# Kernel tuning notes

Measured on AMD Instinct MI355X. Metric: run time of the kernel, lower is better.

The kernel has to match this reference:

```python
import jax, jax.numpy as jnp
import numpy as np

N_NODES = 100000
N_EDGES = 1600000
D_FEAT = 32


def setup_inputs() -> dict:
    key = jax.random.key(0)
    k1, k2, k3 = jax.random.split(key, 3)
    features = jax.random.normal(k1, (N_NODES, D_FEAT), dtype=jnp.float32)
    src = jax.random.randint(k2, (N_EDGES,), 0, N_NODES, dtype=jnp.int64)
    dst = jax.random.randint(k3, (N_EDGES,), 0, N_NODES, dtype=jnp.int64)
    return {"features": features, "src": src, "dst": dst}


def reference(features, src, dst):
    # LightConv with norm='both' (default): symmetric degree normalization.
    n = features.shape[0]
    # out-degrees (number of edges leaving each node)
    deg = jnp.zeros((n,), dtype=features.dtype).at[src].add(1.0)
    # norm = deg^-0.5 with inf -> 0 for isolated nodes
    norm = jnp.where(deg > 0, jax.lax.rsqrt(jnp.maximum(deg, 1.0)), 0.0)[:, None]  # [N,1]
    # pre-scale (norm in ['left','both'])
    x = features * norm
    # message = copy_src, reduce = sum over incoming edges
    agg = jax.ops.segment_sum(x[src], dst, num_segments=n)  # [N,D]
    # post-scale (norm in ['right','both']) -- original reads srcdata['norm'],
    # which is the same per-node norm array for a homogeneous graph.
    return agg * norm
```

## Files before the change

### kernel.cpp

```cpp
#include <hip/hip_runtime.h>

#define D_FEAT 32
#define NPB 256
#define NPB_SHIFT 8
#define KMAX 512
#define BPART 512
#define TPART 256
#define SRC_BITS 17
#define SRC_MASK 0x1FFFF
#define CAPI 6144
#define CAP 2048


__global__ __launch_bounds__(TPART) void partition_atomic(const int* __restrict__ src,
                                                          const int* __restrict__ dst,
                                                          int* __restrict__ cntD_g,
                                                          int* __restrict__ cntS_g,
                                                          int* __restrict__ routed_d,
                                                          unsigned char* __restrict__ routed_b,
                                                          int n_edges, int K) {
    __shared__ int hD[KMAX];
    __shared__ int hS[KMAX];
    __shared__ int bD[KMAX];
    __shared__ int bS[KMAX];
    int b = blockIdx.x;
    int tid = threadIdx.x;
    for (int i = tid; i < K; i += TPART) { hD[i] = 0; hS[i] = 0; }
    __syncthreads();
    int chunk = (((n_edges + BPART - 1) / BPART) + 3) & ~3;
    int base = b * chunk;
    int eend = min(base + chunk, n_edges);
    int nvec = (eend > base) ? ((eend - base) >> 2) : 0;
    const int4* d4p = (const int4*)(dst + base);
    const int4* s4p = (const int4*)(src + base);
    for (int i = tid; i < nvec; i += TPART) {
        int4 d4 = d4p[i];
        int4 s4 = s4p[i];
        atomicAdd(&hD[d4.x >> NPB_SHIFT], 1);
        atomicAdd(&hD[d4.y >> NPB_SHIFT], 1);
        atomicAdd(&hD[d4.z >> NPB_SHIFT], 1);
        atomicAdd(&hD[d4.w >> NPB_SHIFT], 1);
        atomicAdd(&hS[s4.x >> NPB_SHIFT], 1);
        atomicAdd(&hS[s4.y >> NPB_SHIFT], 1);
        atomicAdd(&hS[s4.z >> NPB_SHIFT], 1);
        atomicAdd(&hS[s4.w >> NPB_SHIFT], 1);
    }
    for (int e = base + nvec * 4 + tid; e < eend; e += TPART) {
        atomicAdd(&hD[dst[e] >> NPB_SHIFT], 1);
        atomicAdd(&hS[src[e] >> NPB_SHIFT], 1);
    }
    __syncthreads();
    for (int i = tid; i < K; i += TPART) {
        int c = hD[i];
        bD[i] = (c > 0) ? atomicAdd(&cntD_g[i], c) : 0;
        int c2 = hS[i];
        bS[i] = (c2 > 0) ? atomicAdd(&cntS_g[i], c2) : 0;
    }
    __syncthreads();
    for (int i = tid; i < nvec; i += TPART) {
        int4 d4 = d4p[i];
        int4 s4 = s4p[i];
        int dv[4] = {d4.x, d4.y, d4.z, d4.w};
        int sv[4] = {s4.x, s4.y, s4.z, s4.w};
        #pragma unroll
        for (int u = 0; u < 4; u++) {
            int d = dv[u], s = sv[u];
            int kd = d >> NPB_SHIFT;
            int pos = atomicAdd(&bD[kd], 1);
            routed_d[(size_t)kd * CAPI + min(pos, CAPI - 1)] = ((d & (NPB - 1)) << SRC_BITS) | s;
            int ks = s >> NPB_SHIFT;
            int ps = atomicAdd(&bS[ks], 1);
            routed_b[(size_t)ks * CAPI + min(ps, CAPI - 1)] = (unsigned char)(s & (NPB - 1));
        }
    }
    for (int e = base + nvec * 4 + tid; e < eend; e += TPART) {
        int d = dst[e], s = src[e];
        int kd = d >> NPB_SHIFT;
        int pos = atomicAdd(&bD[kd], 1);
        routed_d[(size_t)kd * CAPI + min(pos, CAPI - 1)] = ((d & (NPB - 1)) << SRC_BITS) | s;
        int ks = s >> NPB_SHIFT;
        int ps = atomicAdd(&bS[ks], 1);
        routed_b[(size_t)ks * CAPI + min(ps, CAPI - 1)] = (unsigned char)(s & (NPB - 1));
    }
}

__global__ __launch_bounds__(256) void count_norm(const unsigned char* __restrict__ routed_b,
                                                  const int* __restrict__ cntS_g,
                                                  float* __restrict__ norm,
                                                  int n_nodes, int K) {
    __shared__ int bins[NPB];
    int k = blockIdx.x;
    int tid = threadIdx.x;
    bins[tid] = 0;
    __syncthreads();
    int beg = k * CAPI;
    int cnt = min(cntS_g[k], CAPI);
    for (int j = tid; j < cnt; j += 256)
        atomicAdd(&bins[routed_b[beg + j]], 1);
    __syncthreads();
    int node = (k << NPB_SHIFT) + tid;
    if (node < n_nodes) {
        int d = bins[tid];
        norm[node] = d > 0 ? rsqrtf((float)d) : 0.0f;
    }
}

__global__ __launch_bounds__(1024) void fused_gather(const float4* __restrict__ feat4,
                                                     const int* __restrict__ routed_d,
                                                     const int* __restrict__ cntD_g,
                                                     const float* __restrict__ norm,
                                                     float4* __restrict__ out4,
                                                     int n_nodes, int K) {
    __shared__ int sbuf[CAP];
    __shared__ int ssort[CAP];
    __shared__ int bins[NPB];
    __shared__ int sc[NPB];
    __shared__ int off[NPB + 1];
    __shared__ int cur[NPB];
    int k = blockIdx.x;
    int tid = threadIdx.x;
    int g = tid >> 5;
    int lane = tid & 31;
    int sub = lane >> 3;
    int il  = lane & 7;
    int kbase = k << NPB_SHIFT;

    int beg = k * CAPI;
    int total = min(cntD_g[k], CAPI);

    float4 acc[8];
    #pragma unroll
    for (int ii = 0; ii < 8; ii++) acc[ii] = make_float4(0.f, 0.f, 0.f, 0.f);

    for (int cb = 0; cb < total; cb += CAP) {
        int n = min(CAP, total - cb);
        __syncthreads();
        for (int i = tid; i < n; i += 1024) sbuf[i] = routed_d[beg + cb + i];
        if (tid < NPB) bins[tid] = 0;
        __syncthreads();
        for (int i = tid; i < n; i += 1024) atomicAdd(&bins[sbuf[i] >> SRC_BITS], 1);
        __syncthreads();
        if (tid < NPB) sc[tid] = bins[tid];
        __syncthreads();
        for (int st = 1; st < NPB; st <<= 1) {
            int v = (tid < NPB && tid >= st) ? sc[tid - st] : 0;
            __syncthreads();
            if (tid < NPB) sc[tid] += v;
            __syncthreads();
        }
        if (tid < NPB) {
            int ex = sc[tid] - bins[tid];
            off[tid] = ex;
            cur[tid] = ex;
        }
        if (tid == NPB - 1) off[NPB] = sc[NPB - 1];
        __syncthreads();
        for (int i = tid; i < n; i += 1024) {
            int p = sbuf[i];
            int pos = atomicAdd(&cur[p >> SRC_BITS], 1);
            ssort[pos] = p & SRC_MASK;
        }
        __syncthreads();
        #pragma unroll
        for (int ii = 0; ii < 8; ii++) {
            int dl = g + (ii << 5);
            int u0 = off[dl], u1 = off[dl + 1];
            float4 a = acc[ii];
            int u = u0;
            for (; u + 8 <= u1; u += 8) {
                int s0 = ssort[u + sub];
                int s1 = ssort[u + 4 + sub];
                float4 f0 = feat4[(size_t)s0 * 8 + il];
                float4 f1 = feat4[(size_t)s1 * 8 + il];
                float w0 = norm[s0];
                float w1 = norm[s1];
                a.x += f0.x * w0 + f1.x * w1;
                a.y += f0.y * w0 + f1.y * w1;
                a.z += f0.z * w0 + f1.z * w1;
                a.w += f0.w * w0 + f1.w * w1;
            }
            for (; u < u1; u += 4) {
                if (u + sub < u1) {
                    int s = ssort[u + sub];
                    float4 f = feat4[(size_t)s * 8 + il];
                    float w = norm[s];
                    a.x += f.x * w; a.y += f.y * w; a.z += f.z * w; a.w += f.w * w;
                }
            }
            acc[ii] = a;
        }
    }

    #pragma unroll
    for (int ii = 0; ii < 8; ii++) {
        float4 a = acc[ii];
        a.x += __shfl_xor(a.x, 8, 32);  a.y += __shfl_xor(a.y, 8, 32);
        a.z += __shfl_xor(a.z, 8, 32);  a.w += __shfl_xor(a.w, 8, 32);
        a.x += __shfl_xor(a.x, 16, 32); a.y += __shfl_xor(a.y, 16, 32);
        a.z += __shfl_xor(a.z, 16, 32); a.w += __shfl_xor(a.w, 16, 32);
        int node = kbase + g + (ii << 5);
        if (node < n_nodes && lane < 8) {
            float nv = norm[node];
            a.x *= nv; a.y *= nv; a.z *= nv; a.w *= nv;
            out4[(size_t)node * 8 + il] = a;
        }
    }
}


__global__ void deg_kernel(const int* __restrict__ src, int* __restrict__ deg, int n_edges) {
    int e = blockIdx.x * blockDim.x + threadIdx.x;
    if (e < n_edges) atomicAdd(&deg[src[e]], 1);
}

__global__ void norm_kernel(const int* __restrict__ deg, float* __restrict__ norm, int n_nodes) {
    int i = blockIdx.x * blockDim.x + threadIdx.x;
    if (i < n_nodes) {
        int d = deg[i];
        norm[i] = d > 0 ? rsqrtf((float)d) : 0.0f;
    }
}

__global__ void scatter_kernel(const float* __restrict__ feat,
                               const int* __restrict__ src,
                               const int* __restrict__ dst,
                               const float* __restrict__ norm,
                               float* __restrict__ out, int n_edges) {
    int t = blockIdx.x * blockDim.x + threadIdx.x;
    int e = t >> 5;
    int d = t & 31;
    if (e < n_edges) {
        int s  = src[e];
        int dd = dst[e];
        float v = feat[s * D_FEAT + d] * norm[s];
        atomicAdd(&out[dd * D_FEAT + d], v);
    }
}

__global__ void post_scale_kernel(float4* __restrict__ out4,
                                  const float* __restrict__ norm, int n4) {
    int t = blockIdx.x * blockDim.x + threadIdx.x;
    if (t < n4) {
        float nv = norm[t >> 3];
        float4 v = out4[t];
        v.x *= nv; v.y *= nv; v.z *= nv; v.w *= nv;
        out4[t] = v;
    }
}


extern "C" void kernel_launch(void* const* d_in, const int* in_sizes, int n_in,
                              void* d_out, int out_size, void* d_ws, size_t ws_size,
                              hipStream_t stream) {
    const float* feat = (const float*)d_in[0];
    const int*   src  = (const int*)d_in[1];
    const int*   dst  = (const int*)d_in[2];
    float* out = (float*)d_out;

    const int n_nodes = in_sizes[0] / D_FEAT;
    const int n_edges = in_sizes[1];
    const int B = 256;

    const int K = (n_nodes + NPB - 1) >> NPB_SHIFT;

    auto align256 = [](size_t x) { return (x + 255) & ~(size_t)255; };
    size_t off = 0;
    size_t cnt_off    = off; off = align256(off + (size_t)2 * K * sizeof(int));
    size_t norm_off   = off; off = align256(off + (size_t)n_nodes * sizeof(float));
    size_t routd_off  = off; off = align256(off + (size_t)K * CAPI * sizeof(int));
    size_t routb_off  = off; off = align256(off + (size_t)K * CAPI * sizeof(unsigned char));
    size_t needed = off;

    bool ok = (ws_size >= needed) && (K <= KMAX) && (n_nodes <= (1 << SRC_BITS));

    if (ok) {
        int*   cntD_g          = (int*)((char*)d_ws + cnt_off);
        int*   cntS_g          = cntD_g + K;
        float* norm            = (float*)((char*)d_ws + norm_off);
        int*   routed_d        = (int*)((char*)d_ws + routd_off);
        unsigned char* routed_b = (unsigned char*)((char*)d_ws + routb_off);

        hipMemsetAsync(cntD_g, 0, (size_t)2 * K * sizeof(int), stream);
        partition_atomic<<<BPART, TPART, 0, stream>>>(src, dst, cntD_g, cntS_g,
                                                      routed_d, routed_b, n_edges, K);
        count_norm<<<K, 256, 0, stream>>>(routed_b, cntS_g, norm, n_nodes, K);
        fused_gather<<<K, 1024, 0, stream>>>((const float4*)feat, routed_d, cntD_g,
                                             norm, (float4*)out, n_nodes, K);
    } else {
        int*   deg  = (int*)d_ws;
        float* norm = (float*)((char*)d_ws + (((size_t)n_nodes * sizeof(int) + 255) & ~(size_t)255));

        hipMemsetAsync(deg, 0, (size_t)n_nodes * sizeof(int), stream);
        hipMemsetAsync(d_out, 0, (size_t)out_size * sizeof(float), stream);

        deg_kernel<<<(n_edges + B - 1) / B, B, 0, stream>>>(src, deg, n_edges);
        norm_kernel<<<(n_nodes + B - 1) / B, B, 0, stream>>>(deg, norm, n_nodes);

        long long total = (long long)n_edges * 32;
        int grid = (int)((total + B - 1) / B);
        scatter_kernel<<<grid, B, 0, stream>>>(feat, src, dst, norm, out, n_edges);

        int n4 = out_size / 4;
        post_scale_kernel<<<(n4 + B - 1) / B, B, 0, stream>>>((float4*)out, norm, n4);
    }
}
```

Measured before the change: 184.3 us.

## Split fused gather into prescale, bucket sort to CSR, and warp-per-node gather

Replaces the monolithic per-bucket fused gather (1024-thread blocks, one per 256-node bucket) with three kernels. A prescale kernel multiplies features by norm once, a sort kernel writes each bucket's sorted source indices and per-node row ranges to global memory, and a warp-per-node CSR gather sums prescaled rows. This removes the per-edge norm load and frees the gather from the bucket block's shared memory and syncs, giving many more small blocks for latency hiding. The cost is two extra launches and extra global traffic for the prescaled feature copy and the sorted index arrays.

```diff
diff --git a/kernel.cpp b/kernel.cpp
--- a/kernel.cpp
+++ b/kernel.cpp
@@ -9,7 +9,6 @@
 #define SRC_BITS 17
 #define SRC_MASK 0x1FFFF
 #define CAPI 6144
-#define CAP 2048
 
 
 __global__ __launch_bounds__(TPART) void partition_atomic(const int* __restrict__ src,
@@ -105,106 +104,96 @@
     }
 }
 
-__global__ __launch_bounds__(1024) void fused_gather(const float4* __restrict__ feat4,
-                                                     const int* __restrict__ routed_d,
-                                                     const int* __restrict__ cntD_g,
-                                                     const float* __restrict__ norm,
-                                                     float4* __restrict__ out4,
-                                                     int n_nodes, int K) {
-    __shared__ int sbuf[CAP];
-    __shared__ int ssort[CAP];
+__global__ void prescale_kernel(const float4* __restrict__ feat4,
+                                const float* __restrict__ norm,
+                                float4* __restrict__ feat_s4, int n4) {
+    int t = blockIdx.x * blockDim.x + threadIdx.x;
+    if (t < n4) {
+        float nv = norm[t >> 3];
+        float4 v = feat4[t];
+        v.x *= nv; v.y *= nv; v.z *= nv; v.w *= nv;
+        feat_s4[t] = v;
+    }
+}
+
+__global__ __launch_bounds__(1024) void sort_bucket(const int* __restrict__ routed_d,
+                                                    const int* __restrict__ cntD_g,
+                                                    int* __restrict__ sorted_src,
+                                                    int* __restrict__ row_beg,
+                                                    int* __restrict__ row_end,
+                                                    int n_nodes, int K) {
     __shared__ int bins[NPB];
     __shared__ int sc[NPB];
-    __shared__ int off[NPB + 1];
     __shared__ int cur[NPB];
     int k = blockIdx.x;
     int tid = threadIdx.x;
-    int g = tid >> 5;
-    int lane = tid & 31;
-    int sub = lane >> 3;
-    int il  = lane & 7;
-    int kbase = k << NPB_SHIFT;
-
     int beg = k * CAPI;
     int total = min(cntD_g[k], CAPI);
-
-    float4 acc[8];
-    #pragma unroll
-    for (int ii = 0; ii < 8; ii++) acc[ii] = make_float4(0.f, 0.f, 0.f, 0.f);
-
-    for (int cb = 0; cb < total; cb += CAP) {
-        int n = min(CAP, total - cb);
+    if (tid < NPB) bins[tid] = 0;
+    __syncthreads();
+    for (int i = tid; i < total; i += 1024)
+        atomicAdd(&bins[routed_d[beg + i] >> SRC_BITS], 1);
+    __syncthreads();
+    if (tid < NPB) sc[tid] = bins[tid];
+    __syncthreads();
+    for (int st = 1; st < NPB; st <<= 1) {
+        int v = (tid < NPB && tid >= st) ? sc[tid - st] : 0;
         __syncthreads();
-        for (int i = tid; i < n; i += 1024) sbuf[i] = routed_d[beg + cb + i];
-        if (tid < NPB) bins[tid] = 0;
+        if (tid < NPB) sc[tid] += v;
         __syncthreads();
-        for (int i = tid; i < n; i += 1024) atomicAdd(&bins[sbuf[i] >> SRC_BITS], 1);
-        __syncthreads();
-        if (tid < NPB) sc[tid] = bins[tid];
-        __syncthreads();
-        for (int st = 1; st < NPB; st <<= 1) {
-            int v = (tid < NPB && tid >= st) ? sc[tid - st] : 0;
-            __syncthreads();
-            if (tid < NPB) sc[tid] += v;
-            __syncthreads();
+    }
+    if (tid < NPB) {
+        int ex = sc[tid] - bins[tid];
+        cur[tid] = ex;
+        int node = (k << NPB_SHIFT) + tid;
+        if (node < n_nodes) {
+            row_beg[node] = beg + ex;
+            row_end[node] = beg + sc[tid];
         }
-        if (tid < NPB) {
-            int ex = sc[tid] - bins[tid];
-            off[tid] = ex;
-            cur[tid] = ex;
+    }
+    __syncthreads();
+    for (int i = tid; i < total; i += 1024) {
+        int p = routed_d[beg + i];
+        int pos = atomicAdd(&cur[p >> SRC_BITS], 1);
+        sorted_src[beg + pos] = p & SRC_MASK;
+    }
+}
+
+__global__ __launch_bounds__(256) void csr_gather(const float* __restrict__ feat_s,
+                                                  const int* __restrict__ sorted_src,
+                                                  const int* __restrict__ row_beg,
+                                                  const int* __restrict__ row_end,
+                                                  const float* __restrict__ norm,
+                                                  float* __restrict__ out, int n_nodes) {
+    int t = blockIdx.x * blockDim.x + threadIdx.x;
+    int node = t >> 5;
+    int lane = t & 31;
+    if (node >= n_nodes) return;
+    int beg = row_beg[node];
+    int end = row_end[node];
+    float acc = 0.0f;
+    for (int base = beg; base < end; base += 32) {
+        int idx = min(base + lane, end - 1);
+        int sv = sorted_src[idx];
+        int m = min(32, end - base);
+        int u = 0;
+        for (; u + 3 < m; u += 4) {
+            int s0 = __shfl(sv, u,     32);
+            int s1 = __shfl(sv, u + 1, 32);
+            int s2 = __shfl(sv, u + 2, 32);
+            int s3 = __shfl(sv, u + 3, 32);
+            float a0 = feat_s[s0 * D_FEAT + lane];
+            float a1 = feat_s[s1 * D_FEAT + lane];
+            float a2 = feat_s[s2 * D_FEAT + lane];
+            float a3 = feat_s[s3 * D_FEAT + lane];
+            acc += (a0 + a1) + (a2 + a3);
         }
-        if (tid == NPB - 1) off[NPB] = sc[NPB - 1];
-        __syncthreads();
-        for (int i = tid; i < n; i += 1024) {
-            int p = sbuf[i];
-            int pos = atomicAdd(&cur[p >> SRC_BITS], 1);
-            ssort[pos] = p & SRC_MASK;
+        for (; u < m; u++) {
+            int s0 = __shfl(sv, u, 32);
+            acc += feat_s[s0 * D_FEAT + lane];
         }
-        __syncthreads();
-        #pragma unroll
-        for (int ii = 0; ii < 8; ii++) {
-            int dl = g + (ii << 5);
-            int u0 = off[dl], u1 = off[dl + 1];
-            float4 a = acc[ii];
-            int u = u0;
-            for (; u + 8 <= u1; u += 8) {
-                int s0 = ssort[u + sub];
-                int s1 = ssort[u + 4 + sub];
-                float4 f0 = feat4[(size_t)s0 * 8 + il];
-                float4 f1 = feat4[(size_t)s1 * 8 + il];
-                float w0 = norm[s0];
-                float w1 = norm[s1];
-                a.x += f0.x * w0 + f1.x * w1;
-                a.y += f0.y * w0 + f1.y * w1;
-                a.z += f0.z * w0 + f1.z * w1;
-                a.w += f0.w * w0 + f1.w * w1;
-            }
-            for (; u < u1; u += 4) {
-                if (u + sub < u1) {
-                    int s = ssort[u + sub];
-                    float4 f = feat4[(size_t)s * 8 + il];
-                    float w = norm[s];
-                    a.x += f.x * w; a.y += f.y * w; a.z += f.z * w; a.w += f.w * w;
-                }
-            }
-            acc[ii] = a;
-        }
-    }
-
-    #pragma unroll
-    for (int ii = 0; ii < 8; ii++) {
-        float4 a = acc[ii];
-        a.x += __shfl_xor(a.x, 8, 32);  a.y += __shfl_xor(a.y, 8, 32);
-        a.z += __shfl_xor(a.z, 8, 32);  a.w += __shfl_xor(a.w, 8, 32);
-        a.x += __shfl_xor(a.x, 16, 32); a.y += __shfl_xor(a.y, 16, 32);
-        a.z += __shfl_xor(a.z, 16, 32); a.w += __shfl_xor(a.w, 16, 32);
-        int node = kbase + g + (ii << 5);
-        if (node < n_nodes && lane < 8) {
-            float nv = norm[node];
-            a.x *= nv; a.y *= nv; a.z *= nv; a.w *= nv;
-            out4[(size_t)node * 8 + il] = a;
-        }
-    }
+    }
+    out[(size_t)node * D_FEAT + lane] = acc * norm[node];
 }
 
 
@@ -269,6 +258,10 @@
     size_t norm_off   = off; off = align256(off + (size_t)n_nodes * sizeof(float));
     size_t routd_off  = off; off = align256(off + (size_t)K * CAPI * sizeof(int));
     size_t routb_off  = off; off = align256(off + (size_t)K * CAPI * sizeof(unsigned char));
+    size_t feats_off  = off; off = align256(off + (size_t)n_nodes * D_FEAT * sizeof(float));
+    size_t sortd_off  = off; off = align256(off + (size_t)K * CAPI * sizeof(int));
+    size_t rbeg_off   = off; off = align256(off + (size_t)n_nodes * sizeof(int));
+    size_t rend_off   = off; off = align256(off + (size_t)n_nodes * sizeof(int));
     size_t needed = off;
 
     bool ok = (ws_size >= needed) && (K <= KMAX) && (n_nodes <= (1 << SRC_BITS));
@@ -279,13 +272,24 @@
         float* norm            = (float*)((char*)d_ws + norm_off);
         int*   routed_d        = (int*)((char*)d_ws + routd_off);
         unsigned char* routed_b = (unsigned char*)((char*)d_ws + routb_off);
+        float* feat_s          = (float*)((char*)d_ws + feats_off);
+        int*   sorted_src      = (int*)((char*)d_ws + sortd_off);
+        int*   row_beg         = (int*)((char*)d_ws + rbeg_off);
+        int*   row_end         = (int*)((char*)d_ws + rend_off);
 
         hipMemsetAsync(cntD_g, 0, (size_t)2 * K * sizeof(int), stream);
         partition_atomic<<<BPART, TPART, 0, stream>>>(src, dst, cntD_g, cntS_g,
                                                       routed_d, routed_b, n_edges, K);
         count_norm<<<K, 256, 0, stream>>>(routed_b, cntS_g, norm, n_nodes, K);
-        fused_gather<<<K, 1024, 0, stream>>>((const float4*)feat, routed_d, cntD_g,
-                                             norm, (float4*)out, n_nodes, K);
+        int n4 = n_nodes * (D_FEAT / 4);
+        prescale_kernel<<<(n4 + B - 1) / B, B, 0, stream>>>((const float4*)feat, norm,
+                                                            (float4*)feat_s, n4);
+        sort_bucket<<<K, 1024, 0, stream>>>(routed_d, cntD_g, sorted_src,
+                                            row_beg, row_end, n_nodes, K);
+        long long total = (long long)n_nodes * 32;
+        int grid = (int)((total + B - 1) / B);
+        csr_gather<<<grid, B, 0, stream>>>(feat_s, sorted_src, row_beg, row_end,
+                                           norm, out, n_nodes);
     } else {
         int*   deg  = (int*)d_ws;
         float* norm = (float*)((char*)d_ws + (((size_t)n_nodes * sizeof(int) + 255) & ~(size_t)255));
```

Result: faster. 169.2 us (-8.2%).
